# Kernel optimization log

Hardware: AMD Instinct MI355X
Metric: run time of the kernel (lower is better)

## Reference

```python
import jax, jax.numpy as jnp
import numpy as np

# Box3dEncoder(cube_bbox_size=[64,64,8], add_occupancy_flag=False)
CUBE = (64, 64, 8)
LOW = (-32, -32, -4)          # low_bound = -res//2
MAXV = 8                      # quad clipped by 4 half-planes has <= 8 verts
VOXEL_SIZE = 0.4
B, N = 4, 16

_OFFSETS = np.array([[0, 0, 0], [1, 0, 0], [1, 1, 0], [0, 1, 0],
                     [0, 0, 1], [1, 0, 1], [1, 1, 1], [0, 1, 1]], np.float32)


def setup_inputs() -> dict:
    key = jax.random.key(0)
    k0, k1, k2, k3 = jax.random.split(key, 4)
    cxy = jax.random.uniform(k0, (B, N, 2), minval=-10.0, maxval=10.0)
    cz = jax.random.uniform(k1, (B, N, 1), minval=-1.0, maxval=1.0)
    dims = jax.random.uniform(k2, (B, N, 3), minval=1.0, maxval=4.0)
    yaw = jax.random.uniform(k3, (B, N), minval=-np.pi, maxval=np.pi)
    unit = jnp.asarray(_OFFSETS) - 0.5                      # [8,3] centered unit cube
    local = unit[None, None] * dims[:, :, None, :]          # [B,N,8,3]
    c, s = jnp.cos(yaw)[..., None], jnp.sin(yaw)[..., None]
    x = local[..., 0] * c - local[..., 1] * s
    y = local[..., 0] * s + local[..., 1] * c
    center = jnp.concatenate([cxy, cz], axis=-1)            # [B,N,3]
    corners3d = jnp.stack([x, y, local[..., 2]], axis=-1) + center[:, :, None, :]
    neck_voxel_sizes = jnp.full((B, 3), VOXEL_SIZE, dtype=jnp.float32)
    return {"corners3d": corners3d.astype(jnp.float32),
            "neck_voxel_sizes": neck_voxel_sizes}


def _clip_one(verts, count, a, b, c):
    # Sutherland-Hodgman clip of a convex polygon (padded to MAXV) by a*x+b*y+c >= 0
    idx = jnp.arange(MAXV)
    valid = idx < count
    nxt_i = jnp.where(idx + 1 < count, idx + 1, 0)
    cur, nxt = verts, verts[nxt_i]
    dc = a * cur[:, 0] + b * cur[:, 1] + c
    dn = a * nxt[:, 0] + b * nxt[:, 1] + c
    denom = dc - dn
    t = dc / jnp.where(jnp.abs(denom) < 1e-12, 1.0, denom)
    ip = cur + t[:, None] * (nxt - cur)                     # edge/plane intersection
    emit_ip = valid & ((dc >= 0) != (dn >= 0))
    emit_nx = valid & (dn >= 0)
    outs = jnp.stack([ip, nxt], axis=1).reshape(2 * MAXV, 2)
    ov = jnp.stack([emit_ip, emit_nx], axis=1).reshape(2 * MAXV)
    order = jnp.argsort(~ov)                                # stable: valid first, in order
    return outs[order][:MAXV], jnp.sum(ov).astype(jnp.int32)


def _clipped_rect_area(poly4, x0, x1, y0, y1):
    # area of (convex) quad poly4 clipped to axis-aligned rect [x0,x1]x[y0,y1]
    verts = jnp.zeros((MAXV, 2), poly4.dtype).at[:4].set(poly4)
    count = jnp.int32(4)
    for a, b, c in ((1.0, 0.0, -x0), (-1.0, 0.0, x1), (0.0, 1.0, -y0), (0.0, -1.0, y1)):
        verts, count = _clip_one(verts, count, a, b, c)
    idx = jnp.arange(MAXV)
    valid = idx < count
    nxt = jnp.where(idx + 1 < count, idx + 1, 0)
    cr = verts[:, 0] * verts[nxt, 1] - verts[nxt, 0] * verts[:, 1]
    return 0.5 * jnp.abs(jnp.sum(jnp.where(valid, cr, 0.0)))


def _quad_area(p):  # [4,2] shoelace
    x, y = p[:, 0], p[:, 1]
    return 0.5 * jnp.abs(jnp.sum(x * jnp.roll(y, -1) - jnp.roll(x, -1) * y))


def _forward(corners3d, neck_voxel_sizes):
    vs = neck_voxel_sizes[0]                                # source uses sample 0 only
    vox_vol = vs[0] * vs[1] * vs[2]
    ii, jj, kk = jnp.meshgrid(jnp.arange(LOW[0], LOW[0] + CUBE[0]),
                              jnp.arange(LOW[1], LOW[1] + CUBE[1]),
                              jnp.arange(LOW[2], LOW[2] + CUBE[2]), indexing='ij')
    ijk = jnp.stack([ii, jj, kk], -1).reshape(-1, 3).astype(corners3d.dtype)  # [V,3]
    lo = ijk * vs
    hi = (ijk + 1.0) * vs
    vox_bounds = jnp.concatenate([lo, hi], axis=-1)         # [V,6] x0 y0 z0 x1 y1 z1

    # heading from BEV corners (faithful: atan2(c0.y-c3.y, c0.x-c3.x))
    heading = jnp.arctan2(corners3d[:, :, 0, 1] - corners3d[:, :, 3, 1],
                          corners3d[:, :, 0, 0] - corners3d[:, :, 3, 0])
    enc = jnp.stack([jnp.sin(heading), jnp.cos(heading)], axis=-1)  # [B,N,2]

    def pair(vb, box):  # vb:[6], box:[8,3] -> (intersection volume, 3D IoU)
        x0, y0, z0, x1, y1, z1 = vb
        poly = box[:4, :2]
        area = _clipped_rect_area(poly, x0, x1, y0, y1)
        zb0, zb1 = box[:, 2].min(), box[:, 2].max()
        zov = jnp.maximum(jnp.minimum(z1, zb1) - jnp.maximum(z0, zb0), 0.0)
        inter = area * zov
        box_vol = _quad_area(poly) * (zb1 - zb0)
        iou = inter / (vox_vol + box_vol - inter + 1e-9)
        return inter, iou

    per_vox = jax.vmap(pair, in_axes=(None, 0))             # over N boxes
    per_grid = jax.vmap(per_vox, in_axes=(0, None))         # over V voxels
    inter, iou = jax.vmap(lambda boxes: per_grid(vox_bounds, boxes))(corners3d)  # [B,V,N]

    idx = jnp.argmax(iou, axis=-1)                          # [B,V]
    inter_sel = jnp.take_along_axis(inter, idx[..., None], axis=-1)[..., 0]
    mask = inter_sel > 0.5 * vox_vol                        # [B,V]
    enc_sel = jax.vmap(lambda e, i: e[i])(enc, idx)         # [B,V,2]
    cond = jnp.where(mask[..., None], enc_sel, 0.0)
    return cond.reshape(-1, 2)                              # jcat over batch -> [B*V,2]


def reference(corners3d, neck_voxel_sizes):
    return _forward(corners3d, neck_voxel_sizes)
```

## Files before the change

### kernel.cpp

```cpp
#include <hip/hip_runtime.h>
#include <math.h>

#define NBOX 16
#define GX 64
#define GY 64
#define GZ 8
#define NVOX (GX * GY * GZ)
#define BLK 256
#define WAVES 4
#define BOXES_PER_WAVE (NBOX / WAVES)
#define BLOCKS_PER_BATCH (NVOX / 64)


#define EMIT_SLOT(K, PX, PY) \
    q##K##x = (_c && oc == K) ? (PX) : q##K##x; \
    q##K##y = (_c && oc == K) ? (PY) : q##K##y;

#define EMITC(NSL, COND, PX, PY) do { const bool _c = (COND); \
    EMIT_SLOT(0, PX, PY) EMIT_SLOT(1, PX, PY) EMIT_SLOT(2, PX, PY) \
    EMIT_SLOT(3, PX, PY) \
    if ((NSL) > 4) { EMIT_SLOT(4, PX, PY) } \
    if ((NSL) > 5) { EMIT_SLOT(5, PX, PY) } \
    if ((NSL) > 6) { EMIT_SLOT(6, PX, PY) } \
    if ((NSL) > 7) { EMIT_SLOT(7, PX, PY) } \
    oc += _c ? 1 : 0; } while (0)

#define CLIP_EDGE(E, NE, NSL) do { \
    const bool  _cv = (E) < cnt; \
    const bool  _wr = !((E) + 1 < cnt); \
    const float _cx = i##E##x, _cy = i##E##y; \
    const float _nx = _wr ? i0x : i##NE##x; \
    const float _ny = _wr ? i0y : i##NE##y; \
    const float _dc = pa * _cx + pb * _cy + pc; \
    const float _dn = pa * _nx + pb * _ny + pc; \
    float _dm = _dc - _dn; \
    _dm = (fabsf(_dm) < 1e-12f) ? 1.0f : _dm; \
    const float _tt  = _dc / _dm; \
    const float _ipx = _cx + _tt * (_nx - _cx); \
    const float _ipy = _cy + _tt * (_ny - _cy); \
    { const bool _e1 = _cv && ((_dc >= 0.0f) != (_dn >= 0.0f)); EMITC(NSL, _e1, _ipx, _ipy); } \
    { const bool _e2 = _cv && (_dn >= 0.0f);                    EMITC(NSL, _e2, _nx, _ny); } \
} while (0)

#define STAGE_DECL_Q() \
    float q0x = 0.0f, q0y = 0.0f, q1x = 0.0f, q1y = 0.0f, \
          q2x = 0.0f, q2y = 0.0f, q3x = 0.0f, q3y = 0.0f, \
          q4x = 0.0f, q4y = 0.0f, q5x = 0.0f, q5y = 0.0f, \
          q6x = 0.0f, q6y = 0.0f, q7x = 0.0f, q7y = 0.0f; \
    int oc = 0;

#define COPY_Q_TO_I() \
    i0x = q0x; i0y = q0y; i1x = q1x; i1y = q1y; \
    i2x = q2x; i2y = q2y; i3x = q3x; i3y = q3y; \
    i4x = q4x; i4y = q4y; i5x = q5x; i5y = q5y; \
    i6x = q6x; i6y = q6y; i7x = q7x; i7y = q7y; \
    cnt = oc;

#define SHOE(E, NE) { \
    const bool  _v  = (E) < cnt; \
    const bool  _wr = !((E) + 1 < cnt); \
    const float _nx = _wr ? i0x : i##NE##x; \
    const float _ny = _wr ? i0y : i##NE##y; \
    const float _cr = i##E##x * _ny - _nx * i##E##y; \
    ssum += _v ? _cr : 0.0f; }

__global__ __launch_bounds__(BLK, 4) void box3d_encoder_kernel(
    const float* __restrict__ corners,
    const float* __restrict__ vsizes,
    float* __restrict__ out)
{
    __shared__ float s_px[NBOX][4], s_py[NBOX][4];
    __shared__ float s_zb0[NBOX], s_zb1[NBOX], s_qa[NBOX];
    __shared__ float s_sin[NBOX], s_cos[NBOX];
    __shared__ float s_ax0[NBOX], s_ax1[NBOX], s_ay0[NBOX], s_ay1[NBOX];
    __shared__ float s_biou[WAVES][64];
    __shared__ float s_bint[WAVES][64];
    __shared__ int   s_bidx[WAVES][64];

    const int b     = blockIdx.x >> 9;
    const int vbase = (blockIdx.x & (BLOCKS_PER_BATCH - 1)) << 6;
    const int t     = threadIdx.x;
    const int w     = t >> 6;
    const int lane  = t & 63;

    const float vs0 = vsizes[0], vs1 = vsizes[1], vs2 = vsizes[2];
    const float vox_vol = vs0 * vs1 * vs2;

    if (t < NBOX) {
        const float* c8 = corners + ((size_t)b * NBOX + t) * 8 * 3;
        float px[4], py[4];
        float zmin = c8[2], zmax = c8[2];
        #pragma unroll
        for (int k = 0; k < 8; k++) {
            float z = c8[k * 3 + 2];
            zmin = fminf(zmin, z);
            zmax = fmaxf(zmax, z);
        }
        #pragma unroll
        for (int k = 0; k < 4; k++) { px[k] = c8[k * 3 + 0]; py[k] = c8[k * 3 + 1]; }

        float sum = 0.0f;
        #pragma unroll
        for (int k = 0; k < 4; k++) {
            int n = (k + 1) & 3;
            sum += px[k] * py[n] - px[n] * py[k];
        }
        s_qa[t] = 0.5f * fabsf(sum);

        float h = atan2f(py[0] - py[3], px[0] - px[3]);
        s_sin[t] = sinf(h);
        s_cos[t] = cosf(h);

        s_zb0[t] = zmin;
        s_zb1[t] = zmax;

        float ax0 = px[0], ax1 = px[0], ay0 = py[0], ay1 = py[0];
        #pragma unroll
        for (int k = 1; k < 4; k++) {
            ax0 = fminf(ax0, px[k]); ax1 = fmaxf(ax1, px[k]);
            ay0 = fminf(ay0, py[k]); ay1 = fmaxf(ay1, py[k]);
        }
        s_ax0[t] = ax0; s_ax1[t] = ax1; s_ay0[t] = ay0; s_ay1[t] = ay1;

        #pragma unroll
        for (int k = 0; k < 4; k++) { s_px[t][k] = px[k]; s_py[t][k] = py[k]; }
    }
    __syncthreads();

    const int v  = vbase + lane;
    const int iz = v & 7;
    const int iy = (v >> 3) & 63;
    const int ix = v >> 9;
    const float fi = (float)(ix - 32);
    const float fj = (float)(iy - 32);
    const float fk = (float)(iz - 4);
    const float x0 = fi * vs0, x1 = (fi + 1.0f) * vs0;
    const float y0 = fj * vs1, y1 = (fj + 1.0f) * vs1;
    const float z0 = fk * vs2, z1 = (fk + 1.0f) * vs2;

    float best_iou   = -1.0f;
    float best_inter = 0.0f;
    int   best_idx   = 0;

    #pragma unroll 1
    for (int nn = 0; nn < BOXES_PER_WAVE; nn++) {
        const int n = (w << 2) + nn;
        float iou = 0.0f, inter = 0.0f;

        const float zb0 = s_zb0[n], zb1 = s_zb1[n];
        const float zov_raw = fminf(z1, zb1) - fmaxf(z0, zb0);
        const bool overlap = (zov_raw > 0.0f)
                          && (s_ax0[n] < x1) && (s_ax1[n] > x0)
                          && (s_ay0[n] < y1) && (s_ay1[n] > y0);

        if (__any((int)overlap)) {
            float i0x = s_px[n][0], i0y = s_py[n][0];
            float i1x = s_px[n][1], i1y = s_py[n][1];
            float i2x = s_px[n][2], i2y = s_py[n][2];
            float i3x = s_px[n][3], i3y = s_py[n][3];
            float i4x = 0.0f, i4y = 0.0f, i5x = 0.0f, i5y = 0.0f;
            float i6x = 0.0f, i6y = 0.0f, i7x = 0.0f, i7y = 0.0f;
            int cnt = 4;

            {
                const float pa = 1.0f, pb = 0.0f, pc = -x0;
                STAGE_DECL_Q();
                CLIP_EDGE(0, 1, 5); CLIP_EDGE(1, 2, 5); CLIP_EDGE(2, 3, 5);
                CLIP_EDGE(3, 4, 5);
                COPY_Q_TO_I();
            }
            {
                const float pa = -1.0f, pb = 0.0f, pc = x1;
                STAGE_DECL_Q();
                CLIP_EDGE(0, 1, 6); CLIP_EDGE(1, 2, 6); CLIP_EDGE(2, 3, 6);
                CLIP_EDGE(3, 4, 6); CLIP_EDGE(4, 5, 6);
                COPY_Q_TO_I();
            }
            {
                const float pa = 0.0f, pb = 1.0f, pc = -y0;
                STAGE_DECL_Q();
                CLIP_EDGE(0, 1, 7); CLIP_EDGE(1, 2, 7); CLIP_EDGE(2, 3, 7);
                CLIP_EDGE(3, 4, 7); CLIP_EDGE(4, 5, 7); CLIP_EDGE(5, 6, 7);
                COPY_Q_TO_I();
            }
            {
                const float pa = 0.0f, pb = -1.0f, pc = y1;
                STAGE_DECL_Q();
                CLIP_EDGE(0, 1, 8); CLIP_EDGE(1, 2, 8); CLIP_EDGE(2, 3, 8);
                CLIP_EDGE(3, 4, 8); CLIP_EDGE(4, 5, 8); CLIP_EDGE(5, 6, 8);
                CLIP_EDGE(6, 7, 8);
                COPY_Q_TO_I();
            }

            float ssum = 0.0f;
            SHOE(0, 1) SHOE(1, 2) SHOE(2, 3) SHOE(3, 4)
            SHOE(4, 5) SHOE(5, 6) SHOE(6, 7) SHOE(7, 7)
            const float area = 0.5f * fabsf(ssum);

            const float zov = fmaxf(zov_raw, 0.0f);
            inter = area * zov;
            const float box_vol = s_qa[n] * (zb1 - zb0);
            iou = inter / (vox_vol + box_vol - inter + 1e-9f);
        }

        if (iou > best_iou) {
            best_iou   = iou;
            best_inter = inter;
            best_idx   = n;
        }
    }

    s_biou[w][lane] = best_iou;
    s_bint[w][lane] = best_inter;
    s_bidx[w][lane] = best_idx;
    __syncthreads();

    if (w == 0) {
        float fiou = s_biou[0][lane];
        float fint = s_bint[0][lane];
        int   fidx = s_bidx[0][lane];
        #pragma unroll
        for (int ww = 1; ww < WAVES; ww++) {
            const float iou2 = s_biou[ww][lane];
            if (iou2 > fiou) {
                fiou = iou2;
                fint = s_bint[ww][lane];
                fidx = s_bidx[ww][lane];
            }
        }
        const bool mask = fint > 0.5f * vox_vol;
        float2 o;
        o.x = mask ? s_sin[fidx] : 0.0f;
        o.y = mask ? s_cos[fidx] : 0.0f;
        reinterpret_cast<float2*>(out)[(size_t)b * NVOX + v] = o;
    }
}

extern "C" void kernel_launch(void* const* d_in, const int* in_sizes, int n_in,
                              void* d_out, int out_size, void* d_ws, size_t ws_size,
                              hipStream_t stream) {
    const float* corners = (const float*)d_in[0];
    const float* vsizes  = (const float*)d_in[1];
    float* out = (float*)d_out;

    const int B = 4;
    dim3 grid(B * BLOCKS_PER_BATCH);
    dim3 block(BLK);
    box3d_encoder_kernel<<<grid, block, 0, stream>>>(corners, vsizes, out);
}
```

Baseline: 70.00 us.

## Share XY polygon clip across Z column and give each wave one box

Each block now covers an 8x8 XY tile with 1024 threads, one wave per box. The 2D polygon clip is computed once per XY cell and reused for all 8 Z slices, since the clipped area does not depend on z. This removes an 8x redundancy in the dominant clipping arithmetic. Per-box IoU and intersection values go to a 64KB shared array, and an argmax over 16 boxes follows. The cost is larger shared memory, 1024-thread blocks and only 256 blocks, which lowers occupancy and parallelism.

```diff
diff --git a/kernel.cpp b/kernel.cpp
--- a/kernel.cpp
+++ b/kernel.cpp
@@ -6,10 +6,8 @@
 #define GY 64
 #define GZ 8
 #define NVOX (GX * GY * GZ)
-#define BLK 256
-#define WAVES 4
-#define BOXES_PER_WAVE (NBOX / WAVES)
-#define BLOCKS_PER_BATCH (NVOX / 64)
+#define BLK 1024
+#define TILES 64
 
 
 #define EMIT_SLOT(K, PX, PY) \
@@ -73,15 +71,16 @@
     __shared__ float s_zb0[NBOX], s_zb1[NBOX], s_qa[NBOX];
     __shared__ float s_sin[NBOX], s_cos[NBOX];
     __shared__ float s_ax0[NBOX], s_ax1[NBOX], s_ay0[NBOX], s_ay1[NBOX];
-    __shared__ float s_biou[WAVES][64];
-    __shared__ float s_bint[WAVES][64];
-    __shared__ int   s_bidx[WAVES][64];
-
-    const int b     = blockIdx.x >> 9;
-    const int vbase = (blockIdx.x & (BLOCKS_PER_BATCH - 1)) << 6;
-    const int t     = threadIdx.x;
-    const int w     = t >> 6;
-    const int lane  = t & 63;
+    __shared__ float s_iou[NBOX][64][8];
+    __shared__ float s_int[NBOX][64][8];
+
+    const int b    = blockIdx.x >> 6;
+    const int tile = blockIdx.x & 63;
+    const int tix  = tile >> 3;
+    const int tiy  = tile & 7;
+    const int t    = threadIdx.x;
+    const int w    = t >> 6;
+    const int lane = t & 63;
 
     const float vs0 = vsizes[0], vs1 = vsizes[1], vs2 = vsizes[2];
     const float vox_vol = vs0 * vs1 * vs2;
@@ -127,112 +126,114 @@
     }
     __syncthreads();
 
-    const int v  = vbase + lane;
-    const int iz = v & 7;
-    const int iy = (v >> 3) & 63;
-    const int ix = v >> 9;
-    const float fi = (float)(ix - 32);
-    const float fj = (float)(iy - 32);
-    const float fk = (float)(iz - 4);
+    const int ixl = lane >> 3;
+    const int iyl = lane & 7;
+    const float fi = (float)(tix * 8 + ixl - 32);
+    const float fj = (float)(tiy * 8 + iyl - 32);
     const float x0 = fi * vs0, x1 = (fi + 1.0f) * vs0;
     const float y0 = fj * vs1, y1 = (fj + 1.0f) * vs1;
-    const float z0 = fk * vs2, z1 = (fk + 1.0f) * vs2;
-
-    float best_iou   = -1.0f;
-    float best_inter = 0.0f;
-    int   best_idx   = 0;
-
-    #pragma unroll 1
-    for (int nn = 0; nn < BOXES_PER_WAVE; nn++) {
-        const int n = (w << 2) + nn;
-        float iou = 0.0f, inter = 0.0f;
-
-        const float zb0 = s_zb0[n], zb1 = s_zb1[n];
-        const float zov_raw = fminf(z1, zb1) - fmaxf(z0, zb0);
-        const bool overlap = (zov_raw > 0.0f)
-                          && (s_ax0[n] < x1) && (s_ax1[n] > x0)
-                          && (s_ay0[n] < y1) && (s_ay1[n] > y0);
-
-        if (__any((int)overlap)) {
-            float i0x = s_px[n][0], i0y = s_py[n][0];
-            float i1x = s_px[n][1], i1y = s_py[n][1];
-            float i2x = s_px[n][2], i2y = s_py[n][2];
-            float i3x = s_px[n][3], i3y = s_py[n][3];
-            float i4x = 0.0f, i4y = 0.0f, i5x = 0.0f, i5y = 0.0f;
-            float i6x = 0.0f, i6y = 0.0f, i7x = 0.0f, i7y = 0.0f;
-            int cnt = 4;
-
-            {
-                const float pa = 1.0f, pb = 0.0f, pc = -x0;
-                STAGE_DECL_Q();
-                CLIP_EDGE(0, 1, 5); CLIP_EDGE(1, 2, 5); CLIP_EDGE(2, 3, 5);
-                CLIP_EDGE(3, 4, 5);
-                COPY_Q_TO_I();
-            }
-            {
-                const float pa = -1.0f, pb = 0.0f, pc = x1;
-                STAGE_DECL_Q();
-                CLIP_EDGE(0, 1, 6); CLIP_EDGE(1, 2, 6); CLIP_EDGE(2, 3, 6);
-                CLIP_EDGE(3, 4, 6); CLIP_EDGE(4, 5, 6);
-                COPY_Q_TO_I();
-            }
-            {
-                const float pa = 0.0f, pb = 1.0f, pc = -y0;
-                STAGE_DECL_Q();
-                CLIP_EDGE(0, 1, 7); CLIP_EDGE(1, 2, 7); CLIP_EDGE(2, 3, 7);
-                CLIP_EDGE(3, 4, 7); CLIP_EDGE(4, 5, 7); CLIP_EDGE(5, 6, 7);
-                COPY_Q_TO_I();
-            }
-            {
-                const float pa = 0.0f, pb = -1.0f, pc = y1;
-                STAGE_DECL_Q();
-                CLIP_EDGE(0, 1, 8); CLIP_EDGE(1, 2, 8); CLIP_EDGE(2, 3, 8);
-                CLIP_EDGE(3, 4, 8); CLIP_EDGE(4, 5, 8); CLIP_EDGE(5, 6, 8);
-                CLIP_EDGE(6, 7, 8);
-                COPY_Q_TO_I();
-            }
-
-            float ssum = 0.0f;
-            SHOE(0, 1) SHOE(1, 2) SHOE(2, 3) SHOE(3, 4)
-            SHOE(4, 5) SHOE(5, 6) SHOE(6, 7) SHOE(7, 7)
-            const float area = 0.5f * fabsf(ssum);
-
-            const float zov = fmaxf(zov_raw, 0.0f);
-            inter = area * zov;
-            const float box_vol = s_qa[n] * (zb1 - zb0);
-            iou = inter / (vox_vol + box_vol - inter + 1e-9f);
-        }
-
-        if (iou > best_iou) {
-            best_iou   = iou;
-            best_inter = inter;
-            best_idx   = n;
-        }
+    const float zgl = -4.0f * vs2, zgh = 4.0f * vs2;
+
+    float riou0 = 0.0f, riou1 = 0.0f, riou2 = 0.0f, riou3 = 0.0f,
+          riou4 = 0.0f, riou5 = 0.0f, riou6 = 0.0f, riou7 = 0.0f;
+    float rint0 = 0.0f, rint1 = 0.0f, rint2 = 0.0f, rint3 = 0.0f,
+          rint4 = 0.0f, rint5 = 0.0f, rint6 = 0.0f, rint7 = 0.0f;
+
+    const float zb0 = s_zb0[w], zb1 = s_zb1[w];
+    const bool overlap = (fminf(zgh, zb1) > fmaxf(zgl, zb0))
+                      && (s_ax0[w] < x1) && (s_ax1[w] > x0)
+                      && (s_ay0[w] < y1) && (s_ay1[w] > y0);
+
+    if (__any((int)overlap)) {
+        float i0x = s_px[w][0], i0y = s_py[w][0];
+        float i1x = s_px[w][1], i1y = s_py[w][1];
+        float i2x = s_px[w][2], i2y = s_py[w][2];
+        float i3x = s_px[w][3], i3y = s_py[w][3];
+        float i4x = 0.0f, i4y = 0.0f, i5x = 0.0f, i5y = 0.0f;
+        float i6x = 0.0f, i6y = 0.0f, i7x = 0.0f, i7y = 0.0f;
+        int cnt = 4;
+
+        {
+            const float pa = 1.0f, pb = 0.0f, pc = -x0;
+            STAGE_DECL_Q();
+            CLIP_EDGE(0, 1, 5); CLIP_EDGE(1, 2, 5); CLIP_EDGE(2, 3, 5);
+            CLIP_EDGE(3, 4, 5);
+            COPY_Q_TO_I();
+        }
+        {
+            const float pa = -1.0f, pb = 0.0f, pc = x1;
+            STAGE_DECL_Q();
+            CLIP_EDGE(0, 1, 6); CLIP_EDGE(1, 2, 6); CLIP_EDGE(2, 3, 6);
+            CLIP_EDGE(3, 4, 6); CLIP_EDGE(4, 5, 6);
+            COPY_Q_TO_I();
+        }
+        {
+            const float pa = 0.0f, pb = 1.0f, pc = -y0;
+            STAGE_DECL_Q();
+            CLIP_EDGE(0, 1, 7); CLIP_EDGE(1, 2, 7); CLIP_EDGE(2, 3, 7);
+            CLIP_EDGE(3, 4, 7); CLIP_EDGE(4, 5, 7); CLIP_EDGE(5, 6, 7);
+            COPY_Q_TO_I();
+        }
+        {
+            const float pa = 0.0f, pb = -1.0f, pc = y1;
+            STAGE_DECL_Q();
+            CLIP_EDGE(0, 1, 8); CLIP_EDGE(1, 2, 8); CLIP_EDGE(2, 3, 8);
+            CLIP_EDGE(3, 4, 8); CLIP_EDGE(4, 5, 8); CLIP_EDGE(5, 6, 8);
+            CLIP_EDGE(6, 7, 8);
+            COPY_Q_TO_I();
+        }
+
+        float ssum = 0.0f;
+        SHOE(0, 1) SHOE(1, 2) SHOE(2, 3) SHOE(3, 4)
+        SHOE(4, 5) SHOE(5, 6) SHOE(6, 7) SHOE(7, 7)
+        const float area = 0.5f * fabsf(ssum);
+
+        const float box_vol = s_qa[w] * (zb1 - zb0);
+
+        #define ZSTEP(Z) { \
+            const float fk  = (float)((Z) - 4); \
+            const float zz0 = fk * vs2, zz1 = (fk + 1.0f) * vs2; \
+            const float zov = fmaxf(fminf(zz1, zb1) - fmaxf(zz0, zb0), 0.0f); \
+            const float inter = area * zov; \
+            rint##Z = inter; \
+            riou##Z = inter / (vox_vol + box_vol - inter + 1e-9f); }
+        ZSTEP(0) ZSTEP(1) ZSTEP(2) ZSTEP(3)
+        ZSTEP(4) ZSTEP(5) ZSTEP(6) ZSTEP(7)
+        #undef ZSTEP
     }
 
-    s_biou[w][lane] = best_iou;
-    s_bint[w][lane] = best_inter;
-    s_bidx[w][lane] = best_idx;
+    reinterpret_cast<float4*>(&s_iou[w][lane][0])[0] =
+        make_float4(riou0, riou1, riou2, riou3);
+    reinterpret_cast<float4*>(&s_iou[w][lane][4])[0] =
+        make_float4(riou4, riou5, riou6, riou7);
+    reinterpret_cast<float4*>(&s_int[w][lane][0])[0] =
+        make_float4(rint0, rint1, rint2, rint3);
+    reinterpret_cast<float4*>(&s_int[w][lane][4])[0] =
+        make_float4(rint4, rint5, rint6, rint7);
     __syncthreads();
 
-    if (w == 0) {
-        float fiou = s_biou[0][lane];
-        float fint = s_bint[0][lane];
-        int   fidx = s_bidx[0][lane];
-        #pragma unroll
-        for (int ww = 1; ww < WAVES; ww++) {
-            const float iou2 = s_biou[ww][lane];
-            if (iou2 > fiou) {
-                fiou = iou2;
-                fint = s_bint[ww][lane];
-                fidx = s_bidx[ww][lane];
-            }
+    if (t < 512) {
+        const int xy = t >> 3;
+        const int z  = t & 7;
+        float fiou = s_iou[0][xy][z];
+        float fint = s_int[0][xy][z];
+        int   fidx = 0;
+        #pragma unroll
+        for (int n = 1; n < NBOX; n++) {
+            const float i2 = s_iou[n][xy][z];
+            const float t2 = s_int[n][xy][z];
+            const bool  g  = i2 > fiou;
+            fiou = g ? i2 : fiou;
+            fint = g ? t2 : fint;
+            fidx = g ? n  : fidx;
         }
         const bool mask = fint > 0.5f * vox_vol;
         float2 o;
         o.x = mask ? s_sin[fidx] : 0.0f;
         o.y = mask ? s_cos[fidx] : 0.0f;
-        reinterpret_cast<float2*>(out)[(size_t)b * NVOX + v] = o;
+        const int ix = tix * 8 + (xy >> 3);
+        const int iy = tiy * 8 + (xy & 7);
+        reinterpret_cast<float2*>(out)[(size_t)b * NVOX + ix * 512 + iy * 8 + z] = o;
     }
 }
 
@@ -244,7 +245,7 @@
     float* out = (float*)d_out;
 
     const int B = 4;
-    dim3 grid(B * BLOCKS_PER_BATCH);
+    dim3 grid(B * TILES);
     dim3 block(BLK);
     box3d_encoder_kernel<<<grid, block, 0, stream>>>(corners, vsizes, out);
 }
```

Measured after the change: 63.14 us. 1.11x faster.
